# Performance work log

Hardware: AMD Instinct MI355X
Metric: run time of the kernel (lower is better)

The kernel has to match this reference:

```python
import jax, jax.numpy as jnp
import numpy as np

T, B, N, D = 32, 8, 256, 512
TAU = 2.0   # LIF membrane time constant
VTH = 1.0   # spike threshold
ALPHA = 4.0 # surrogate-gradient sharpness


def setup_inputs() -> dict:
    key = jax.random.key(0)
    k0, k1, k2 = jax.random.split(key, 3)
    scale = 1.0 / np.sqrt(D)
    return {
        "x": jax.random.normal(k0, (T, B, N, D), jnp.float32),
        "tr_mx": jnp.zeros((B, N, D), jnp.float32),            # initial membrane state
        "W_lif": jax.random.normal(k1, (D, D), jnp.float32) * scale,
        "b_lif": jnp.zeros((D,), jnp.float32),
        "W_rec": jax.random.normal(k2, (D, D), jnp.float32) * scale,  # recon2 weight (d_ff=D -> patch_size=D)
        "b_rec": jnp.zeros((D,), jnp.float32),
    }


def _spike(v):
    # Heaviside forward, sigmoid surrogate backward (standard SNN straight-through)
    s = jax.nn.sigmoid(ALPHA * v)
    return s + jax.lax.stop_gradient((v > 0).astype(v.dtype) - s)


def reference(x, tr_mx, W_lif, b_lif, W_rec, b_rec):
    # MemoryUpdate.replay: tau-decayed LIF recurrence over time, emitting spike gate per step
    inp = jnp.einsum('tbnd,de->tbne', x, W_lif) + b_lif   # [T,B,N,D] input current

    def step(mem, i_t):
        mem = mem + (i_t - mem) / TAU        # leaky integration
        sp = _spike(mem - VTH)               # fire
        mem = mem * (1.0 - sp)               # hard reset
        return mem, sp

    _, sp_seq = jax.lax.scan(step, tr_mx, inp)  # sp_seq: [T,B,N,D]

    g = x * (1.0 - sp_seq)                       # gated residual
    rec_x = jnp.einsum('tbnd,dp->tbnp', g, W_rec) + b_rec  # recon2 on flattened (T*B, N, D)
    return rec_x
```

## Files before the change

### kernel.cpp

```cpp
#include <hip/hip_runtime.h>
#include <hip/hip_bf16.h>


#define TT 32
#define CH 8
#define BB 8
#define NN 256
#define DD 512

typedef __attribute__((ext_vector_type(8))) short short8;
typedef __attribute__((ext_vector_type(4))) float f32x4;

__device__ __forceinline__ unsigned short f2bf(float f) {
    __hip_bfloat16 h = __float2bfloat16(f);
    return *reinterpret_cast<unsigned short*>(&h);
}

__global__ void cast_transpose_wr(const float* __restrict__ Wr,
                                  unsigned short* __restrict__ Wt) {
    int idx = blockIdx.x * 256 + threadIdx.x;
    int d = idx >> 9;
    int p = idx & 511;
    Wt[p * DD + d] = f2bf(Wr[idx]);
}

__global__ __launch_bounds__(512, 4) void lif_phaseA_g4(
    const float* __restrict__ x,
    const float* __restrict__ tr_mx,
    const float* __restrict__ Wl,
    const float* __restrict__ bl,
    unsigned short* __restrict__ gws)
{
    __shared__ __align__(16) float xs[4 * CH * DD];

    const int tid = threadIdx.x;
    const int tq  = tid >> 7;
    const int tl  = tid & 127;
    const int e0  = tl * 4;
    const int tok = blockIdx.x * 4 + tq;
    const size_t base = (size_t)tok * DD;
    const size_t st   = (size_t)BB * NN * DD;

    float acc[CH][4];
    float4 m4 = *reinterpret_cast<const float4*>(&tr_mx[base + e0]);
    float m[4] = {m4.x, m4.y, m4.z, m4.w};

    const float4 blv = *reinterpret_cast<const float4*>(&bl[e0]);
    const float blr[4] = {blv.x, blv.y, blv.z, blv.w};

    #pragma unroll 1
    for (int tg = 0; tg < 4; ++tg) {
        #pragma unroll
        for (int r = 0; r < 8; ++r) {
            const int flat = r * 512 + tid;
            const int q    = flat >> 10;
            const int rem  = flat & 1023;
            const int row  = rem >> 7;
            const int c4   = rem & 127;
            const float4 v = *reinterpret_cast<const float4*>(
                &x[(size_t)(tg * CH + row) * st
                   + (size_t)(blockIdx.x * 4 + q) * DD + c4 * 4]);
            *reinterpret_cast<float4*>(&xs[(q * CH + row) * DD + c4 * 4]) = v;
        }
        __syncthreads();

        #pragma unroll
        for (int i = 0; i < CH; ++i)
            #pragma unroll
            for (int e = 0; e < 4; ++e) acc[i][e] = blr[e];

        const float* xsl = &xs[tq * CH * DD];

        #pragma unroll 2
        for (int d = 0; d < DD; d += 4) {
            const float4 w0 = *reinterpret_cast<const float4*>(&Wl[(size_t)(d + 0) * DD + e0]);
            const float4 w1 = *reinterpret_cast<const float4*>(&Wl[(size_t)(d + 1) * DD + e0]);
            const float4 w2 = *reinterpret_cast<const float4*>(&Wl[(size_t)(d + 2) * DD + e0]);
            const float4 w3 = *reinterpret_cast<const float4*>(&Wl[(size_t)(d + 3) * DD + e0]);
            #pragma unroll
            for (int i = 0; i < CH; ++i) {
                const float4 xv = *reinterpret_cast<const float4*>(&xsl[i * DD + d]);
                acc[i][0] = fmaf(xv.x, w0.x, acc[i][0]);
                acc[i][1] = fmaf(xv.x, w0.y, acc[i][1]);
                acc[i][2] = fmaf(xv.x, w0.z, acc[i][2]);
                acc[i][3] = fmaf(xv.x, w0.w, acc[i][3]);
                acc[i][0] = fmaf(xv.y, w1.x, acc[i][0]);
                acc[i][1] = fmaf(xv.y, w1.y, acc[i][1]);
                acc[i][2] = fmaf(xv.y, w1.z, acc[i][2]);
                acc[i][3] = fmaf(xv.y, w1.w, acc[i][3]);
                acc[i][0] = fmaf(xv.z, w2.x, acc[i][0]);
                acc[i][1] = fmaf(xv.z, w2.y, acc[i][1]);
                acc[i][2] = fmaf(xv.z, w2.z, acc[i][2]);
                acc[i][3] = fmaf(xv.z, w2.w, acc[i][3]);
                acc[i][0] = fmaf(xv.w, w3.x, acc[i][0]);
                acc[i][1] = fmaf(xv.w, w3.y, acc[i][1]);
                acc[i][2] = fmaf(xv.w, w3.z, acc[i][2]);
                acc[i][3] = fmaf(xv.w, w3.w, acc[i][3]);
            }
        }

        #pragma unroll
        for (int i = 0; i < CH; ++i) {
            const int t = tg * CH + i;
            const float4 xv = *reinterpret_cast<const float4*>(&xsl[i * DD + e0]);
            float g[4];
            const float xr[4] = {xv.x, xv.y, xv.z, xv.w};
            #pragma unroll
            for (int e = 0; e < 4; ++e) {
                m[e] = m[e] + (acc[i][e] - m[e]) * 0.5f;
                const float s = (m[e] - 1.0f > 0.0f) ? 1.0f : 0.0f;
                g[e] = (s > 0.0f) ? 0.0f : xr[e];
                m[e] *= (1.0f - s);
            }
            uint2 p;
            p.x = (unsigned)f2bf(g[0]) | ((unsigned)f2bf(g[1]) << 16);
            p.y = (unsigned)f2bf(g[2]) | ((unsigned)f2bf(g[3]) << 16);
            *reinterpret_cast<uint2*>(&gws[((size_t)tok * TT + t) * DD + e0]) = p;
        }
        __syncthreads();
    }
}

__global__ __launch_bounds__(512, 2) void lif_phaseB4(
    const unsigned short* __restrict__ gws,
    const unsigned short* __restrict__ Wt,
    const float* __restrict__ br,
    float* __restrict__ out)
{
    const int tid = threadIdx.x;
    const int w    = tid >> 6;
    const int lane = tid & 63;
    const int hB   = w & 1;
    const int q    = w >> 1;
    const int lcol = lane & 15;
    const int lkg  = lane >> 4;
    const int tA   = hB * 16 + lcol;
    const size_t st = (size_t)BB * NN * DD;
    const int colb = q * 128;
    const int tok0 = blockIdx.x * 2;

    const unsigned short* arow0 = &gws[((size_t)tok0 * TT + tA) * DD];
    const unsigned short* arow1 = &gws[((size_t)(tok0 + 1) * TT + tA) * DD];

    f32x4 acc0[8], acc1[8];
    #pragma unroll
    for (int nt = 0; nt < 8; ++nt) {
        const float b = br[colb + nt * 16 + lcol];
        acc0[nt] = (f32x4){b, b, b, b};
        acc1[nt] = (f32x4){b, b, b, b};
    }

    #pragma unroll 1
    for (int ks = 0; ks < 16; ++ks) {
        const int kb = ks * 32 + lkg * 8;
        const short8 a0 = *reinterpret_cast<const short8*>(&arow0[kb]);
        const short8 a1 = *reinterpret_cast<const short8*>(&arow1[kb]);
        #pragma unroll
        for (int nt = 0; nt < 8; ++nt) {
            const int col = colb + nt * 16 + lcol;
            const short8 bf = *reinterpret_cast<const short8*>(&Wt[(size_t)col * DD + kb]);
            acc0[nt] = __builtin_amdgcn_mfma_f32_16x16x32_bf16(a0, bf, acc0[nt], 0, 0, 0);
            acc1[nt] = __builtin_amdgcn_mfma_f32_16x16x32_bf16(a1, bf, acc1[nt], 0, 0, 0);
        }
    }

    #pragma unroll
    for (int nt = 0; nt < 8; ++nt) {
        const int col = colb + nt * 16 + lcol;
        #pragma unroll
        for (int r = 0; r < 4; ++r) {
            const int t = hB * 16 + lkg * 4 + r;
            out[(size_t)t * st + (size_t)tok0 * DD + col]       = acc0[nt][r];
            out[(size_t)t * st + (size_t)(tok0 + 1) * DD + col] = acc1[nt][r];
        }
    }
}

__global__ __launch_bounds__(128, 4) void lif_phaseA_m(
    const float* __restrict__ x, const float* __restrict__ tr_mx,
    const float* __restrict__ Wl, const float* __restrict__ bl,
    unsigned* __restrict__ gmsk)
{
    __shared__ __align__(16) float xs[CH * 256];

    const int tid = threadIdx.x;
    const int tok = blockIdx.x;
    const int e0  = tid * 4;
    const size_t base = (size_t)tok * DD;
    const size_t st   = (size_t)BB * NN * DD;

    float acc[CH][4];
    float4 m4 = *reinterpret_cast<const float4*>(&tr_mx[base + e0]);
    float m[4] = {m4.x, m4.y, m4.z, m4.w};
    unsigned mc[4] = {0u, 0u, 0u, 0u};
    const float4 blv = *reinterpret_cast<const float4*>(&bl[e0]);
    const float blr[4] = {blv.x, blv.y, blv.z, blv.w};

    #pragma unroll 1
    for (int tg = 0; tg < 4; ++tg) {
        #pragma unroll
        for (int i = 0; i < CH; ++i)
            #pragma unroll
            for (int e = 0; e < 4; ++e) acc[i][e] = blr[e];

        #pragma unroll 1
        for (int h = 0; h < 2; ++h) {
            #pragma unroll
            for (int r = 0; r < 4; ++r) {
                const int flat = r * 128 + tid;
                const int row  = flat >> 6;
                const int c4   = flat & 63;
                const float4 v = *reinterpret_cast<const float4*>(
                    &x[(size_t)(tg * CH + row) * st + base + h * 256 + c4 * 4]);
                *reinterpret_cast<float4*>(&xs[row * 256 + c4 * 4]) = v;
            }
            __syncthreads();

            #pragma unroll 2
            for (int dd_ = 0; dd_ < 256; dd_ += 4) {
                const int d = h * 256 + dd_;
                const float4 w0 = *reinterpret_cast<const float4*>(&Wl[(size_t)(d + 0) * DD + e0]);
                const float4 w1 = *reinterpret_cast<const float4*>(&Wl[(size_t)(d + 1) * DD + e0]);
                const float4 w2 = *reinterpret_cast<const float4*>(&Wl[(size_t)(d + 2) * DD + e0]);
                const float4 w3 = *reinterpret_cast<const float4*>(&Wl[(size_t)(d + 3) * DD + e0]);
                #pragma unroll
                for (int i = 0; i < CH; ++i) {
                    const float4 xv = *reinterpret_cast<const float4*>(&xs[i * 256 + dd_]);
                    acc[i][0] = fmaf(xv.x, w0.x, acc[i][0]);
                    acc[i][1] = fmaf(xv.x, w0.y, acc[i][1]);
                    acc[i][2] = fmaf(xv.x, w0.z, acc[i][2]);
                    acc[i][3] = fmaf(xv.x, w0.w, acc[i][3]);
                    acc[i][0] = fmaf(xv.y, w1.x, acc[i][0]);
                    acc[i][1] = fmaf(xv.y, w1.y, acc[i][1]);
                    acc[i][2] = fmaf(xv.y, w1.z, acc[i][2]);
                    acc[i][3] = fmaf(xv.y, w1.w, acc[i][3]);
                    acc[i][0] = fmaf(xv.z, w2.x, acc[i][0]);
                    acc[i][1] = fmaf(xv.z, w2.y, acc[i][1]);
                    acc[i][2] = fmaf(xv.z, w2.z, acc[i][2]);
                    acc[i][3] = fmaf(xv.z, w2.w, acc[i][3]);
                    acc[i][0] = fmaf(xv.w, w3.x, acc[i][0]);
                    acc[i][1] = fmaf(xv.w, w3.y, acc[i][1]);
                    acc[i][2] = fmaf(xv.w, w3.z, acc[i][2]);
                    acc[i][3] = fmaf(xv.w, w3.w, acc[i][3]);
                }
            }
            __syncthreads();
        }

        #pragma unroll
        for (int i = 0; i < CH; ++i) {
            const int t = tg * CH + i;
            #pragma unroll
            for (int e = 0; e < 4; ++e) {
                m[e] = m[e] + (acc[i][e] - m[e]) * 0.5f;
                const float s = (m[e] - 1.0f > 0.0f) ? 1.0f : 0.0f;
                mc[e] |= (s > 0.0f) ? (1u << t) : 0u;
                m[e] *= (1.0f - s);
            }
        }
    }

    uint4 mv;
    mv.x = mc[0]; mv.y = mc[1]; mv.z = mc[2]; mv.w = mc[3];
    *reinterpret_cast<uint4*>(&gmsk[base + e0]) = mv;
}

template<bool UW>
__global__ __launch_bounds__(256, 2) void lif_phaseB2(
    const float* __restrict__ x, const float* __restrict__ Wr,
    const float* __restrict__ br, const unsigned short* __restrict__ Wt,
    const unsigned* __restrict__ gmsk, float* __restrict__ out)
{
    __shared__ __align__(16) unsigned ms[2 * DD];

    const int tid = threadIdx.x;
    const size_t st = (size_t)BB * NN * DD;
    {
        const uint4 v = *reinterpret_cast<const uint4*>(
            &gmsk[(size_t)blockIdx.x * 2 * DD + tid * 4]);
        *reinterpret_cast<uint4*>(&ms[tid * 4]) = v;
    }
    __syncthreads();

    const int wv   = tid >> 6;
    const int lane = tid & 63;
    const int qB   = wv >> 1;
    const int hB   = wv & 1;
    const int lcol = lane & 15;
    const int lkg  = lane >> 4;
    const int tA   = hB * 16 + lcol;
    const size_t baseB = (size_t)(blockIdx.x * 2 + qB) * DD;
    const unsigned* mq = &ms[qB * DD];
    const float* xrow = &x[(size_t)tA * st + baseB];

    #pragma unroll 1
    for (int pass = 0; pass < 4; ++pass) {
        const int colb = pass * 128;
        f32x4 acc[8];
        #pragma unroll
        for (int nt = 0; nt < 8; ++nt) {
            const float b = br[colb + nt * 16 + lcol];
            acc[nt] = (f32x4){b, b, b, b};
        }
        #pragma unroll 1
        for (int ks = 0; ks < 16; ++ks) {
            const int kb = ks * 32 + lkg * 8;
            const float4 x0 = *reinterpret_cast<const float4*>(&xrow[kb]);
            const float4 x1 = *reinterpret_cast<const float4*>(&xrow[kb + 4]);
            const uint4 m0 = *reinterpret_cast<const uint4*>(&mq[kb]);
            const uint4 m1 = *reinterpret_cast<const uint4*>(&mq[kb + 4]);
            short8 a;
            a[0] = (short)f2bf(((m0.x >> tA) & 1u) ? 0.0f : x0.x);
            a[1] = (short)f2bf(((m0.y >> tA) & 1u) ? 0.0f : x0.y);
            a[2] = (short)f2bf(((m0.z >> tA) & 1u) ? 0.0f : x0.z);
            a[3] = (short)f2bf(((m0.w >> tA) & 1u) ? 0.0f : x0.w);
            a[4] = (short)f2bf(((m1.x >> tA) & 1u) ? 0.0f : x1.x);
            a[5] = (short)f2bf(((m1.y >> tA) & 1u) ? 0.0f : x1.y);
            a[6] = (short)f2bf(((m1.z >> tA) & 1u) ? 0.0f : x1.z);
            a[7] = (short)f2bf(((m1.w >> tA) & 1u) ? 0.0f : x1.w);
            #pragma unroll
            for (int nt = 0; nt < 8; ++nt) {
                const int col = colb + nt * 16 + lcol;
                short8 bf;
                if (UW) {
                    bf = *reinterpret_cast<const short8*>(&Wt[(size_t)col * DD + kb]);
                } else {
                    #pragma unroll
                    for (int j = 0; j < 8; ++j)
                        bf[j] = (short)f2bf(Wr[(size_t)(kb + j) * DD + col]);
                }
                acc[nt] = __builtin_amdgcn_mfma_f32_16x16x32_bf16(a, bf, acc[nt], 0, 0, 0);
            }
        }
        #pragma unroll
        for (int nt = 0; nt < 8; ++nt) {
            const int col = colb + nt * 16 + lcol;
            #pragma unroll
            for (int r = 0; r < 4; ++r) {
                const int t = hB * 16 + lkg * 4 + r;
                out[(size_t)t * st + baseB + col] = acc[nt][r];
            }
        }
    }
}

extern "C" void kernel_launch(void* const* d_in, const int* in_sizes, int n_in,
                              void* d_out, int out_size, void* d_ws, size_t ws_size,
                              hipStream_t stream) {
    const float* x     = (const float*)d_in[0];
    const float* tr_mx = (const float*)d_in[1];
    const float* Wl    = (const float*)d_in[2];
    const float* bl    = (const float*)d_in[3];
    const float* Wr    = (const float*)d_in[4];
    const float* br    = (const float*)d_in[5];
    float* out = (float*)d_out;

    const size_t g_bytes   = (size_t)BB * NN * TT * DD * 2;
    const size_t wt_bytes  = (size_t)DD * DD * 2;
    const size_t msk_bytes = (size_t)BB * NN * DD * 4;

    if (ws_size >= g_bytes + wt_bytes) {
        unsigned short* gws = (unsigned short*)d_ws;
        unsigned short* Wt  = (unsigned short*)((char*)d_ws + g_bytes);
        cast_transpose_wr<<<dim3(1024), dim3(256), 0, stream>>>(Wr, Wt);
        lif_phaseA_g4<<<dim3(BB * NN / 4), dim3(512), 0, stream>>>(x, tr_mx, Wl, bl, gws);
        lif_phaseB4<<<dim3(BB * NN / 2), dim3(512), 0, stream>>>(gws, Wt, br, out);
    } else if (ws_size >= msk_bytes + wt_bytes) {
        unsigned* gmsk = (unsigned*)d_ws;
        unsigned short* Wt = (unsigned short*)((char*)d_ws + msk_bytes);
        cast_transpose_wr<<<dim3(1024), dim3(256), 0, stream>>>(Wr, Wt);
        lif_phaseA_m<<<dim3(BB * NN), dim3(128), 0, stream>>>(x, tr_mx, Wl, bl, gmsk);
        lif_phaseB2<true><<<dim3(BB * NN / 2), dim3(256), 0, stream>>>(x, Wr, br, Wt, gmsk, out);
    } else if (ws_size >= msk_bytes) {
        unsigned* gmsk = (unsigned*)d_ws;
        lif_phaseA_m<<<dim3(BB * NN), dim3(128), 0, stream>>>(x, tr_mx, Wl, bl, gmsk);
        lif_phaseB2<false><<<dim3(BB * NN / 2), dim3(256), 0, stream>>>(x, Wr, br, nullptr, gmsk, out);
    }
}
```

Before: 625.8 us.

## Fuse LIF recurrence and MFMA recon GEMM into one kernel per token group

Merges the phase-A LIF kernel and the phase-B MFMA GEMM into a single kernel. Each block computes gated bf16 activations for 4 tokens, then reads them back (likely from L2) and runs the W_rec GEMM over all 512 output columns in 4 passes. This removes one kernel launch and lets the gws reads hit recently written data. In exchange, occupancy drops (launch bounds change from 4 to 2), and the GEMM part now uses 512 blocks instead of 1024, each doing 4 sequential column passes, so parallelism is lower.

```diff
diff --git a/kernel.cpp b/kernel.cpp
--- a/kernel.cpp
+++ b/kernel.cpp
@@ -24,154 +24,161 @@
     Wt[p * DD + d] = f2bf(Wr[idx]);
 }
 
-__global__ __launch_bounds__(512, 4) void lif_phaseA_g4(
+template<bool UW>
+__global__ __launch_bounds__(512, 2) void lif_fused(
     const float* __restrict__ x,
     const float* __restrict__ tr_mx,
     const float* __restrict__ Wl,
     const float* __restrict__ bl,
-    unsigned short* __restrict__ gws)
+    const float* __restrict__ Wr,
+    const float* __restrict__ br,
+    const unsigned short* __restrict__ Wt,
+    unsigned short* __restrict__ gws,
+    float* __restrict__ out)
 {
     __shared__ __align__(16) float xs[4 * CH * DD];
 
     const int tid = threadIdx.x;
-    const int tq  = tid >> 7;
-    const int tl  = tid & 127;
-    const int e0  = tl * 4;
-    const int tok = blockIdx.x * 4 + tq;
-    const size_t base = (size_t)tok * DD;
-    const size_t st   = (size_t)BB * NN * DD;
-
-    float acc[CH][4];
-    float4 m4 = *reinterpret_cast<const float4*>(&tr_mx[base + e0]);
-    float m[4] = {m4.x, m4.y, m4.z, m4.w};
-
-    const float4 blv = *reinterpret_cast<const float4*>(&bl[e0]);
-    const float blr[4] = {blv.x, blv.y, blv.z, blv.w};
-
-    #pragma unroll 1
-    for (int tg = 0; tg < 4; ++tg) {
-        #pragma unroll
-        for (int r = 0; r < 8; ++r) {
-            const int flat = r * 512 + tid;
-            const int q    = flat >> 10;
-            const int rem  = flat & 1023;
-            const int row  = rem >> 7;
-            const int c4   = rem & 127;
-            const float4 v = *reinterpret_cast<const float4*>(
-                &x[(size_t)(tg * CH + row) * st
-                   + (size_t)(blockIdx.x * 4 + q) * DD + c4 * 4]);
-            *reinterpret_cast<float4*>(&xs[(q * CH + row) * DD + c4 * 4]) = v;
-        }
-        __syncthreads();
-
-        #pragma unroll
-        for (int i = 0; i < CH; ++i)
-            #pragma unroll
-            for (int e = 0; e < 4; ++e) acc[i][e] = blr[e];
-
-        const float* xsl = &xs[tq * CH * DD];
-
-        #pragma unroll 2
-        for (int d = 0; d < DD; d += 4) {
-            const float4 w0 = *reinterpret_cast<const float4*>(&Wl[(size_t)(d + 0) * DD + e0]);
-            const float4 w1 = *reinterpret_cast<const float4*>(&Wl[(size_t)(d + 1) * DD + e0]);
-            const float4 w2 = *reinterpret_cast<const float4*>(&Wl[(size_t)(d + 2) * DD + e0]);
-            const float4 w3 = *reinterpret_cast<const float4*>(&Wl[(size_t)(d + 3) * DD + e0]);
+    const size_t st = (size_t)BB * NN * DD;
+
+    {
+        const int tq  = tid >> 7;
+        const int tl  = tid & 127;
+        const int e0  = tl * 4;
+        const int tok = blockIdx.x * 4 + tq;
+        const size_t base = (size_t)tok * DD;
+
+        float acc[CH][4];
+        float4 m4 = *reinterpret_cast<const float4*>(&tr_mx[base + e0]);
+        float m[4] = {m4.x, m4.y, m4.z, m4.w};
+
+        const float4 blv = *reinterpret_cast<const float4*>(&bl[e0]);
+        const float blr[4] = {blv.x, blv.y, blv.z, blv.w};
+
+        #pragma unroll 1
+        for (int tg = 0; tg < 4; ++tg) {
+            #pragma unroll
+            for (int r = 0; r < 8; ++r) {
+                const int flat = r * 512 + tid;
+                const int q    = flat >> 10;
+                const int rem  = flat & 1023;
+                const int row  = rem >> 7;
+                const int c4   = rem & 127;
+                const float4 v = *reinterpret_cast<const float4*>(
+                    &x[(size_t)(tg * CH + row) * st
+                       + (size_t)(blockIdx.x * 4 + q) * DD + c4 * 4]);
+                *reinterpret_cast<float4*>(&xs[(q * CH + row) * DD + c4 * 4]) = v;
+            }
+            __syncthreads();
+
+            #pragma unroll
+            for (int i = 0; i < CH; ++i)
+                #pragma unroll
+                for (int e = 0; e < 4; ++e) acc[i][e] = blr[e];
+
+            const float* xsl = &xs[tq * CH * DD];
+
+            #pragma unroll 2
+            for (int d = 0; d < DD; d += 4) {
+                const float4 w0 = *reinterpret_cast<const float4*>(&Wl[(size_t)(d + 0) * DD + e0]);
+                const float4 w1 = *reinterpret_cast<const float4*>(&Wl[(size_t)(d + 1) * DD + e0]);
+                const float4 w2 = *reinterpret_cast<const float4*>(&Wl[(size_t)(d + 2) * DD + e0]);
+                const float4 w3 = *reinterpret_cast<const float4*>(&Wl[(size_t)(d + 3) * DD + e0]);
+                #pragma unroll
+                for (int i = 0; i < CH; ++i) {
+                    const float4 xv = *reinterpret_cast<const float4*>(&xsl[i * DD + d]);
+                    acc[i][0] = fmaf(xv.x, w0.x, acc[i][0]);
+                    acc[i][1] = fmaf(xv.x, w0.y, acc[i][1]);
+                    acc[i][2] = fmaf(xv.x, w0.z, acc[i][2]);
+                    acc[i][3] = fmaf(xv.x, w0.w, acc[i][3]);
+                    acc[i][0] = fmaf(xv.y, w1.x, acc[i][0]);
+                    acc[i][1] = fmaf(xv.y, w1.y, acc[i][1]);
+                    acc[i][2] = fmaf(xv.y, w1.z, acc[i][2]);
+                    acc[i][3] = fmaf(xv.y, w1.w, acc[i][3]);
+                    acc[i][0] = fmaf(xv.z, w2.x, acc[i][0]);
+                    acc[i][1] = fmaf(xv.z, w2.y, acc[i][1]);
+                    acc[i][2] = fmaf(xv.z, w2.z, acc[i][2]);
+                    acc[i][3] = fmaf(xv.z, w2.w, acc[i][3]);
+                    acc[i][0] = fmaf(xv.w, w3.x, acc[i][0]);
+                    acc[i][1] = fmaf(xv.w, w3.y, acc[i][1]);
+                    acc[i][2] = fmaf(xv.w, w3.z, acc[i][2]);
+                    acc[i][3] = fmaf(xv.w, w3.w, acc[i][3]);
+                }
+            }
+
             #pragma unroll
             for (int i = 0; i < CH; ++i) {
-                const float4 xv = *reinterpret_cast<const float4*>(&xsl[i * DD + d]);
-                acc[i][0] = fmaf(xv.x, w0.x, acc[i][0]);
-                acc[i][1] = fmaf(xv.x, w0.y, acc[i][1]);
-                acc[i][2] = fmaf(xv.x, w0.z, acc[i][2]);
-                acc[i][3] = fmaf(xv.x, w0.w, acc[i][3]);
-                acc[i][0] = fmaf(xv.y, w1.x, acc[i][0]);
-                acc[i][1] = fmaf(xv.y, w1.y, acc[i][1]);
-                acc[i][2] = fmaf(xv.y, w1.z, acc[i][2]);
-                acc[i][3] = fmaf(xv.y, w1.w, acc[i][3]);
-                acc[i][0] = fmaf(xv.z, w2.x, acc[i][0]);
-                acc[i][1] = fmaf(xv.z, w2.y, acc[i][1]);
-                acc[i][2] = fmaf(xv.z, w2.z, acc[i][2]);
-                acc[i][3] = fmaf(xv.z, w2.w, acc[i][3]);
-                acc[i][0] = fmaf(xv.w, w3.x, acc[i][0]);
-                acc[i][1] = fmaf(xv.w, w3.y, acc[i][1]);
-                acc[i][2] = fmaf(xv.w, w3.z, acc[i][2]);
-                acc[i][3] = fmaf(xv.w, w3.w, acc[i][3]);
-            }
-        }
-
-        #pragma unroll
-        for (int i = 0; i < CH; ++i) {
-            const int t = tg * CH + i;
-            const float4 xv = *reinterpret_cast<const float4*>(&xsl[i * DD + e0]);
-            float g[4];
-            const float xr[4] = {xv.x, xv.y, xv.z, xv.w};
-            #pragma unroll
-            for (int e = 0; e < 4; ++e) {
-                m[e] = m[e] + (acc[i][e] - m[e]) * 0.5f;
-                const float s = (m[e] - 1.0f > 0.0f) ? 1.0f : 0.0f;
-                g[e] = (s > 0.0f) ? 0.0f : xr[e];
-                m[e] *= (1.0f - s);
-            }
-            uint2 p;
-            p.x = (unsigned)f2bf(g[0]) | ((unsigned)f2bf(g[1]) << 16);
-            p.y = (unsigned)f2bf(g[2]) | ((unsigned)f2bf(g[3]) << 16);
-            *reinterpret_cast<uint2*>(&gws[((size_t)tok * TT + t) * DD + e0]) = p;
-        }
-        __syncthreads();
-    }
-}
-
-__global__ __launch_bounds__(512, 2) void lif_phaseB4(
-    const unsigned short* __restrict__ gws,
-    const unsigned short* __restrict__ Wt,
-    const float* __restrict__ br,
-    float* __restrict__ out)
-{
-    const int tid = threadIdx.x;
-    const int w    = tid >> 6;
-    const int lane = tid & 63;
-    const int hB   = w & 1;
-    const int q    = w >> 1;
-    const int lcol = lane & 15;
-    const int lkg  = lane >> 4;
-    const int tA   = hB * 16 + lcol;
-    const size_t st = (size_t)BB * NN * DD;
-    const int colb = q * 128;
-    const int tok0 = blockIdx.x * 2;
-
-    const unsigned short* arow0 = &gws[((size_t)tok0 * TT + tA) * DD];
-    const unsigned short* arow1 = &gws[((size_t)(tok0 + 1) * TT + tA) * DD];
-
-    f32x4 acc0[8], acc1[8];
-    #pragma unroll
-    for (int nt = 0; nt < 8; ++nt) {
-        const float b = br[colb + nt * 16 + lcol];
-        acc0[nt] = (f32x4){b, b, b, b};
-        acc1[nt] = (f32x4){b, b, b, b};
-    }
-
-    #pragma unroll 1
-    for (int ks = 0; ks < 16; ++ks) {
-        const int kb = ks * 32 + lkg * 8;
-        const short8 a0 = *reinterpret_cast<const short8*>(&arow0[kb]);
-        const short8 a1 = *reinterpret_cast<const short8*>(&arow1[kb]);
-        #pragma unroll
-        for (int nt = 0; nt < 8; ++nt) {
-            const int col = colb + nt * 16 + lcol;
-            const short8 bf = *reinterpret_cast<const short8*>(&Wt[(size_t)col * DD + kb]);
-            acc0[nt] = __builtin_amdgcn_mfma_f32_16x16x32_bf16(a0, bf, acc0[nt], 0, 0, 0);
-            acc1[nt] = __builtin_amdgcn_mfma_f32_16x16x32_bf16(a1, bf, acc1[nt], 0, 0, 0);
-        }
-    }
-
-    #pragma unroll
-    for (int nt = 0; nt < 8; ++nt) {
-        const int col = colb + nt * 16 + lcol;
-        #pragma unroll
-        for (int r = 0; r < 4; ++r) {
-            const int t = hB * 16 + lkg * 4 + r;
-            out[(size_t)t * st + (size_t)tok0 * DD + col]       = acc0[nt][r];
-            out[(size_t)t * st + (size_t)(tok0 + 1) * DD + col] = acc1[nt][r];
+                const int t = tg * CH + i;
+                const float4 xv = *reinterpret_cast<const float4*>(&xsl[i * DD + e0]);
+                float g[4];
+                const float xr[4] = {xv.x, xv.y, xv.z, xv.w};
+                #pragma unroll
+                for (int e = 0; e < 4; ++e) {
+                    m[e] = m[e] + (acc[i][e] - m[e]) * 0.5f;
+                    const float s = (m[e] - 1.0f > 0.0f) ? 1.0f : 0.0f;
+                    g[e] = (s > 0.0f) ? 0.0f : xr[e];
+                    m[e] *= (1.0f - s);
+                }
+                uint2 p;
+                p.x = (unsigned)f2bf(g[0]) | ((unsigned)f2bf(g[1]) << 16);
+                p.y = (unsigned)f2bf(g[2]) | ((unsigned)f2bf(g[3]) << 16);
+                *reinterpret_cast<uint2*>(&gws[((size_t)tok * TT + t) * DD + e0]) = p;
+            }
+            __syncthreads();
+        }
+    }
+    __syncthreads();
+
+    {
+        const int w    = tid >> 6;
+        const int lane = tid & 63;
+        const int tq2  = w >> 1;
+        const int hB   = w & 1;
+        const int lcol = lane & 15;
+        const int lkg  = lane >> 4;
+        const int tA   = hB * 16 + lcol;
+        const int tokB = blockIdx.x * 4 + tq2;
+
+        const unsigned short* arow = &gws[((size_t)tokB * TT + tA) * DD];
+
+        #pragma unroll 1
+        for (int pass = 0; pass < 4; ++pass) {
+            const int colb = pass * 128;
+            f32x4 acc[8];
+            #pragma unroll
+            for (int nt = 0; nt < 8; ++nt) {
+                const float b = br[colb + nt * 16 + lcol];
+                acc[nt] = (f32x4){b, b, b, b};
+            }
+
+            #pragma unroll 1
+            for (int ks = 0; ks < 16; ++ks) {
+                const int kb = ks * 32 + lkg * 8;
+                const short8 a = *reinterpret_cast<const short8*>(&arow[kb]);
+                #pragma unroll
+                for (int nt = 0; nt < 8; ++nt) {
+                    const int col = colb + nt * 16 + lcol;
+                    short8 bf;
+                    if (UW) {
+                        bf = *reinterpret_cast<const short8*>(&Wt[(size_t)col * DD + kb]);
+                    } else {
+                        #pragma unroll
+                        for (int j = 0; j < 8; ++j)
+                            bf[j] = (short)f2bf(Wr[(size_t)(kb + j) * DD + col]);
+                    }
+                    acc[nt] = __builtin_amdgcn_mfma_f32_16x16x32_bf16(a, bf, acc[nt], 0, 0, 0);
+                }
+            }
+
+            #pragma unroll
+            for (int nt = 0; nt < 8; ++nt) {
+                const int col = colb + nt * 16 + lcol;
+                #pragma unroll
+                for (int r = 0; r < 4; ++r) {
+                    const int t = hB * 16 + lkg * 4 + r;
+                    out[(size_t)t * st + (size_t)tokB * DD + col] = acc[nt][r];
+                }
+            }
         }
     }
 }
@@ -363,8 +370,8 @@
         unsigned short* gws = (unsigned short*)d_ws;
         unsigned short* Wt  = (unsigned short*)((char*)d_ws + g_bytes);
         cast_transpose_wr<<<dim3(1024), dim3(256), 0, stream>>>(Wr, Wt);
-        lif_phaseA_g4<<<dim3(BB * NN / 4), dim3(512), 0, stream>>>(x, tr_mx, Wl, bl, gws);
-        lif_phaseB4<<<dim3(BB * NN / 2), dim3(512), 0, stream>>>(gws, Wt, br, out);
+        lif_fused<true><<<dim3(BB * NN / 4), dim3(512), 0, stream>>>(
+            x, tr_mx, Wl, bl, Wr, br, Wt, gws, out);
     } else if (ws_size >= msk_bytes + wt_bytes) {
         unsigned* gmsk = (unsigned*)d_ws;
         unsigned short* Wt = (unsigned short*)((char*)d_ws + msk_bytes);
```

After: 665.9 us. 6.4% more time.
